# Kernel tuning notes

Measured on AMD Instinct MI355X. Metric: run time of the kernel, lower is better.

## Reference

```python
import jax, jax.numpy as jnp
import numpy as np

B, D, I = 16384, 2048, 2048


def setup_inputs() -> dict:
    key = jax.random.key(0)
    kx, kh, kw = jax.random.split(key, 3)
    x = jax.random.normal(kx, (B, I), dtype=jnp.float32)
    h = jax.random.normal(kh, (B, D), dtype=jnp.float32)
    # input projection weight (Linear, no bias): [d_model, inpt_size]
    W_ih = jax.random.normal(kw, (D, I), dtype=jnp.float32) * 0.02
    # orthogonal-ish hidden transition (torch uses an SVD-orthogonal block),
    # well-conditioned so the inverse is exact and stable
    rng = np.random.default_rng(0)
    q, _ = np.linalg.qr(rng.standard_normal((D, D)).astype(np.float64))
    W_hh = jnp.asarray(q, dtype=jnp.float32)
    W_inv = jnp.asarray(np.linalg.inv(q), dtype=jnp.float32)  # buffer self.inv
    return {"x": x, "h": h, "W_ih": W_ih, "W_hh": W_hh, "W_inv": W_inv}


def reference(x, h, W_ih, W_hh, W_inv):
    # outs = inpt_linear(x) : [B, D]
    outs = jnp.einsum("bi,di->bd", x, W_ih)
    not_trig = outs[..., -1] >= -1.0          # [B]
    h_last = h[..., -1]                        # [B]
    m_fwd = ((h_last > 0) & not_trig)[..., None]   # forward rotation branch
    m_inv = ((h_last < 0) & not_trig)[..., None]   # inverse rotation branch
    m_pass = (~not_trig)[..., None]                # passthrough branch
    hW = h @ W_hh   # torch.matmul(h, weight_hh) (no transpose)
    hI = h @ W_inv  # torch.matmul(h, inv)
    zero = jnp.zeros((), dtype=outs.dtype)
    return (outs
            + jnp.where(m_fwd, hW, zero)
            + jnp.where(m_inv, hI, zero)
            + jnp.where(m_pass, h, zero))
```

## Files before the change

kernel.cpp:

```cpp
#include <hip/hip_runtime.h>
#include <hip/hip_bf16.h>
#include <stdint.h>

#define B_ROWS 16384
#define DIM 2048
#define BK 64
#define NT 96

typedef float f32x4 __attribute__((ext_vector_type(4)));
typedef short bf16x8 __attribute__((ext_vector_type(8)));
using u16 = unsigned short;
using u32 = unsigned int;

__device__ __forceinline__ u32 pack_bf2(float a, float b) {
  __hip_bfloat162 t = __float22bfloat162_rn(float2{a, b});
  union { __hip_bfloat162 b2; u32 u; } cv;
  cv.b2 = t;
  return cv.u;
}

__device__ __forceinline__ u16 f2bf_rne(float f) {
  union { float f; u32 u; } v;
  v.f = f;
  u32 u = v.u;
  u32 r = u + 0x7FFFu + ((u >> 16) & 1u);
  return (u16)(r >> 16);
}

__device__ __forceinline__ void gload16(const void* g, void* l) {
  __builtin_amdgcn_global_load_lds(
      (const __attribute__((address_space(1))) u32*)g,
      (__attribute__((address_space(3))) u32*)l, 16, 0, 0);
}

__global__ __launch_bounds__(256) void k_prep(
    const float* __restrict__ x, const float* __restrict__ h,
    const float* __restrict__ W_ih, int* __restrict__ flags,
    u16* __restrict__ xb, u16* __restrict__ hF, u16* __restrict__ hI) {
  int row = blockIdx.x * 4 + (threadIdx.x >> 6);
  int lane = threadIdx.x & 63;
  const float* xr = x + (size_t)row * DIM;
  const float* hr = h + (size_t)row * DIM;
  const float* wr = W_ih + (size_t)(DIM - 1) * DIM;
  u16* xbr = xb + (size_t)row * DIM;
  double s = 0.0;
  u32 hp[16];
#pragma unroll
  for (int i = 0; i < 8; ++i) {
    int idx = (i * 64 + lane) * 4;
    f32x4 xv = *(const f32x4*)(xr + idx);
    f32x4 wv = *(const f32x4*)(wr + idx);
    f32x4 hv = *(const f32x4*)(hr + idx);
    s += (double)xv.x * wv.x + (double)xv.y * wv.y +
         (double)xv.z * wv.z + (double)xv.w * wv.w;
    *(uint2*)(xbr + idx) = uint2{pack_bf2(xv.x, xv.y), pack_bf2(xv.z, xv.w)};
    hp[2 * i] = pack_bf2(hv.x, hv.y);
    hp[2 * i + 1] = pack_bf2(hv.z, hv.w);
  }
#pragma unroll
  for (int off = 32; off > 0; off >>= 1) s += __shfl_xor(s, off);
  float hl = hr[DIM - 1];
  int f = (s < -1.0) ? 2 : (hl > 0.f ? 0 : (hl < 0.f ? 1 : 3));
  if (lane == 0) flags[row] = f;
  uint2 z{0u, 0u};
  u16* hFr = hF + (size_t)row * DIM;
  u16* hIr = hI + (size_t)row * DIM;
#pragma unroll
  for (int i = 0; i < 8; ++i) {
    int idx = (i * 64 + lane) * 4;
    uint2 p{hp[2 * i], hp[2 * i + 1]};
    *(uint2*)(hFr + idx) = (f == 0) ? p : z;
    *(uint2*)(hIr + idx) = (f == 1) ? p : z;
  }
}

__global__ __launch_bounds__(256) void k_flags_fb(
    const float* __restrict__ x, const float* __restrict__ h,
    const float* __restrict__ W_ih, int* __restrict__ flags) {
  int row = blockIdx.x * 4 + (threadIdx.x >> 6);
  int lane = threadIdx.x & 63;
  const float* xr = x + (size_t)row * DIM;
  const float* wr = W_ih + (size_t)(DIM - 1) * DIM;
  double s = 0.0;
#pragma unroll
  for (int i = 0; i < 8; ++i) {
    int idx = (i * 64 + lane) * 4;
    f32x4 xv = *(const f32x4*)(xr + idx);
    f32x4 wv = *(const f32x4*)(wr + idx);
    s += (double)xv.x * wv.x + (double)xv.y * wv.y +
         (double)xv.z * wv.z + (double)xv.w * wv.w;
  }
#pragma unroll
  for (int off = 32; off > 0; off >>= 1) s += __shfl_xor(s, off);
  if (lane == 0) {
    float hl = h[(size_t)row * DIM + (DIM - 1)];
    flags[row] = (s < -1.0) ? 2 : (hl > 0.f ? 0 : (hl < 0.f ? 1 : 3));
  }
}

__global__ __launch_bounds__(256) void k_convert(const float* __restrict__ src,
                                                 u16* __restrict__ dst) {
  size_t i = ((size_t)blockIdx.x * 256 + threadIdx.x) * 4;
  f32x4 v = *(const f32x4*)(src + i);
  *(uint2*)(dst + i) = uint2{pack_bf2(v.x, v.y), pack_bf2(v.z, v.w)};
}

__global__ __launch_bounds__(256) void k_transpose(const float* __restrict__ src,
                                                   u16* __restrict__ dst) {
  __shared__ float tile[32][33];
  int k0 = blockIdx.x * 32;
  int n0 = blockIdx.y * 32;
  int tx = threadIdx.x & 31;
  int ty = threadIdx.x >> 5;
#pragma unroll
  for (int i = 0; i < 4; ++i)
    tile[ty + 8 * i][tx] = src[(size_t)(k0 + ty + 8 * i) * DIM + n0 + tx];
  __syncthreads();
#pragma unroll
  for (int i = 0; i < 4; ++i)
    dst[(size_t)(n0 + ty + 8 * i) * DIM + k0 + tx] = f2bf_rne(tile[tx][ty + 8 * i]);
}

__global__ __launch_bounds__(512, 2) void k_gemm8(
    const u16* __restrict__ xb, const u16* __restrict__ hF,
    const u16* __restrict__ hI, const u16* __restrict__ Wih,
    const u16* __restrict__ WhhT, const u16* __restrict__ WinvT,
    const int* __restrict__ flags, const float* __restrict__ h,
    float* __restrict__ out) {
  __shared__ __attribute__((aligned(128))) char smem[131072];

  int o = blockIdx.x;
  int brow = (o >> 3) * 256;
  int bcol = (o & 7) * 256;

  int t = threadIdx.x;
  int lane = t & 63;
  int wave = t >> 6;
  int wr = wave >> 2;
  int wc = wave & 3;

  int sx16 = (((lane & 3) ^ ((lane >> 3) & 3)) << 4);
  int fA = (((lane >> 4) ^ ((lane >> 1) & 3)) << 4);
  int arowbase = wr * 128 + (lane & 15);
  int browbase = wc * 64 + (lane & 15);

  auto stage = [&](int T, int isB, int kk) {
    if (T >= NT) T -= NT;
    int seg = T >> 5;
    int kt = T & 31;
    const u16* mat = isB ? (seg == 0 ? Wih : seg == 1 ? WhhT : WinvT)
                         : (seg == 0 ? xb : seg == 1 ? hF : hI);
    int r0 = isB ? bcol : brow;
    size_t gb = (size_t)(r0 + wave * 32 + (lane >> 2)) * (DIM * 2) +
                (size_t)kt * 128 + (size_t)kk * 64 + (size_t)sx16;
    char* ldst = smem + ((T & 1) << 16) + kk * 32768 + isB * 16384 +
                 (wave * 32) * 64;
    gload16((const char*)mat + gb, ldst);
    gload16((const char*)mat + gb + (size_t)16 * (DIM * 2), ldst + 1024);
  };

  f32x4 acc[8][4] = {};
  bf16x8 aF[8], bF[4];

  stage(0, 0, 0); stage(0, 1, 0);
  stage(0, 0, 1); stage(0, 1, 1);
  stage(1, 0, 0); stage(1, 1, 0);
  asm volatile("s_waitcnt vmcnt(8)" ::: "memory");
  __builtin_amdgcn_s_barrier();

#define PHASE(KK, STT, STKK)                                                   \
  {                                                                            \
    const char* Ab_ = smem + buf + (KK) * 32768;                               \
    _Pragma("unroll") for (int m = 0; m < 4; ++m) {                            \
      aF[m] = *(const bf16x8*)(Ab_ + (arowbase + m * 16) * 64 + fA);           \
      aF[4 + m] = *(const bf16x8*)(Ab_ + (arowbase + 64 + m * 16) * 64 + fA);  \
    }                                                                          \
    _Pragma("unroll") for (int n = 0; n < 4; ++n)                              \
        bF[n] = *(const bf16x8*)(Ab_ + 16384 + (browbase + n * 16) * 64 + fA); \
    stage(STT, 0, STKK);                                                       \
    stage(STT, 1, STKK);                                                       \
    asm volatile("s_waitcnt vmcnt(8)" ::: "memory");                           \
    __builtin_amdgcn_s_barrier();                                              \
    asm volatile("s_waitcnt lgkmcnt(0)" ::: "memory");                         \
    __builtin_amdgcn_sched_barrier(0);                                         \
    __builtin_amdgcn_s_setprio(1);                                             \
    _Pragma("unroll") for (int mh = 0; mh < 2; ++mh)                           \
        _Pragma("unroll") for (int m = 0; m < 4; ++m)                          \
            _Pragma("unroll") for (int n = 0; n < 4; ++n)                      \
                acc[mh * 4 + m][n] = __builtin_amdgcn_mfma_f32_16x16x32_bf16(  \
                    aF[mh * 4 + m], bF[n], acc[mh * 4 + m][n], 0, 0, 0);       \
    __builtin_amdgcn_s_setprio(0);                                             \
  }

#pragma unroll 1
  for (int T = 0; T < NT; ++T) {
    const int buf = (T & 1) << 16;
    PHASE(0, T + 1, 1)
    PHASE(1, T + 2, 0)
  }
#undef PHASE
  asm volatile("s_waitcnt vmcnt(0)" ::: "memory");

#pragma unroll
  for (int mi = 0; mi < 8; ++mi) {
    int rbase = brow + wr * 128 + (mi >> 2) * 64 + (mi & 3) * 16 + (lane >> 4) * 4;
#pragma unroll
    for (int j = 0; j < 4; ++j) {
      int row = rbase + j;
      bool pass = (flags[row] == 2);
#pragma unroll
      for (int n = 0; n < 4; ++n) {
        int col = bcol + wc * 64 + n * 16 + (lane & 15);
        float v = acc[mi][n][j];
        if (pass) v += h[(size_t)row * DIM + col];
        out[(size_t)row * DIM + col] = v;
      }
    }
  }
}

#define BM 128
#define BN 128
__global__ __launch_bounds__(256, 2) void k_gemm_fb(
    const float* __restrict__ x, const float* __restrict__ h,
    const u16* __restrict__ Wih, const u16* __restrict__ WhhT,
    const u16* __restrict__ WinvT, const int* __restrict__ flags,
    float* __restrict__ out) {
  __shared__ char smem[(BM + BN) * BK * 2];
  char* sA = smem;
  char* sB = smem + BM * BK * 2;

  int o = blockIdx.x;
  int swz = (o & 7) * ((int)gridDim.x >> 3) + (o >> 3);
  int brow = (swz >> 4) * BM;
  int bcol = (swz & 15) * BN;

  int t = threadIdx.x;
  int lane = t & 63;
  int wave = t >> 6;
  int wrow = (wave >> 1) * 64;
  int wcol = (wave & 1) * 64;

  f32x4 acc[4][4] = {};
  int sc = t & 15;
  int sr0 = t >> 4;

  int aOff[4][2], bOff[4][2];
#pragma unroll
  for (int m = 0; m < 4; ++m)
#pragma unroll
    for (int kk = 0; kk < 2; ++kk) {
      int ar = wrow + m * 16 + (lane & 15);
      aOff[m][kk] = ar * (BK * 2) + ((kk * 64 + (lane >> 4) * 16) ^ ((ar & 7) << 4));
      int br = wcol + m * 16 + (lane & 15);
      bOff[m][kk] = br * (BK * 2) + ((kk * 64 + (lane >> 4) * 16) ^ ((br & 7) << 4));
    }

#pragma unroll 1
  for (int seg = 0; seg < 3; ++seg) {
    const float* Asrc = (seg == 0) ? x : h;
    const u16* Bsrc = (seg == 0) ? Wih : (seg == 1) ? WhhT : WinvT;
    int want = seg - 1;

    float rmask[8];
#pragma unroll
    for (int i = 0; i < 8; ++i) {
      int r = sr0 + 16 * i;
      rmask[i] = (want < 0 || flags[brow + r] == want) ? 1.f : 0.f;
    }

#pragma unroll 1
    for (int k0 = 0; k0 < DIM; k0 += BK) {
      __syncthreads();
#pragma unroll
      for (int i = 0; i < 8; ++i) {
        int r = sr0 + 16 * i;
        f32x4 v = *(const f32x4*)(Asrc + (size_t)(brow + r) * DIM + k0 + sc * 4);
        float msk = rmask[i];
        int off = r * (BK * 2) + ((sc * 8) ^ ((r & 7) << 4));
        *(uint2*)(sA + off) =
            uint2{pack_bf2(v.x * msk, v.y * msk), pack_bf2(v.z * msk, v.w * msk)};
      }
#pragma unroll
      for (int i = 0; i < 4; ++i) {
        int ch = t + 256 * i;
        int r = ch >> 3;
        int c = ch & 7;
        uint4 v = *(const uint4*)(Bsrc + (size_t)(bcol + r) * DIM + k0 + c * 8);
        int off = r * (BK * 2) + ((c * 16) ^ ((r & 7) << 4));
        *(uint4*)(sB + off) = v;
      }
      __syncthreads();
      bf16x8 aF2[4][2], bF2[4][2];
#pragma unroll
      for (int m = 0; m < 4; ++m)
#pragma unroll
        for (int kk = 0; kk < 2; ++kk) {
          aF2[m][kk] = *(const bf16x8*)(sA + aOff[m][kk]);
          bF2[m][kk] = *(const bf16x8*)(sB + bOff[m][kk]);
        }
#pragma unroll
      for (int kk = 0; kk < 2; ++kk)
#pragma unroll
        for (int m = 0; m < 4; ++m)
#pragma unroll
          for (int n = 0; n < 4; ++n)
            acc[m][n] = __builtin_amdgcn_mfma_f32_16x16x32_bf16(
                aF2[m][kk], bF2[n][kk], acc[m][n], 0, 0, 0);
    }
  }

#pragma unroll
  for (int m = 0; m < 4; ++m) {
    int rbase = brow + wrow + m * 16 + (lane >> 4) * 4;
#pragma unroll
    for (int j = 0; j < 4; ++j) {
      int row = rbase + j;
      bool pass = (flags[row] == 2);
#pragma unroll
      for (int n = 0; n < 4; ++n) {
        int col = bcol + wcol + n * 16 + (lane & 15);
        float v = acc[m][n][j];
        if (pass) v += h[(size_t)row * DIM + col];
        out[(size_t)row * DIM + col] = v;
      }
    }
  }
}

extern "C" void kernel_launch(void* const* d_in, const int* in_sizes, int n_in,
                              void* d_out, int out_size, void* d_ws, size_t ws_size,
                              hipStream_t stream) {
  const float* x = (const float*)d_in[0];
  const float* h = (const float*)d_in[1];
  const float* W_ih = (const float*)d_in[2];
  const float* W_hh = (const float*)d_in[3];
  const float* W_inv = (const float*)d_in[4];
  float* out = (float*)d_out;

  char* ws = (char*)d_ws;
  int* flags = (int*)ws;
  u16* WihB = (u16*)(ws + (64 << 10));
  u16* WhhT = WihB + (size_t)DIM * DIM;
  u16* WinvT = WhhT + (size_t)DIM * DIM;
  u16* xb = WinvT + (size_t)DIM * DIM;
  u16* hF = xb + (size_t)B_ROWS * DIM;
  u16* hI = hF + (size_t)B_ROWS * DIM;
  size_t need = (size_t)(64 << 10) + 3ull * DIM * DIM * 2 + 3ull * B_ROWS * DIM * 2;

  k_convert<<<(DIM * DIM / 4) / 256, 256, 0, stream>>>(W_ih, WihB);
  k_transpose<<<dim3(DIM / 32, DIM / 32), 256, 0, stream>>>(W_hh, WhhT);
  k_transpose<<<dim3(DIM / 32, DIM / 32), 256, 0, stream>>>(W_inv, WinvT);

  if (ws_size >= need) {
    k_prep<<<B_ROWS / 4, 256, 0, stream>>>(x, h, W_ih, flags, xb, hF, hI);
    k_gemm8<<<(B_ROWS / 256) * (DIM / 256), 512, 0, stream>>>(
        xb, hF, hI, WihB, WhhT, WinvT, flags, h, out);
  } else {
    k_flags_fb<<<B_ROWS / 4, 256, 0, stream>>>(x, h, W_ih, flags);
    k_gemm_fb<<<(B_ROWS / BM) * (DIM / BN), 256, 0, stream>>>(x, h, WihB, WhhT,
                                                              WinvT, flags, out);
  }
}
```

Baseline: 518.2 us.

## Shrink GEMM tile to 256x128 with 4 waves and triple-buffered K=32 phases

Changes the main GEMM from 512-thread 256x256 tiles with double-buffered K=64 stages to 256-thread 256x128 tiles. Each phase now stages K=32 slices into a 3-deep LDS ring of 24KB buffers. It also adds a block-index swizzle so neighbouring blocks share row or column panels. The aim is smaller LDS use (72KB) to allow two blocks per CU, plus more blocks for load balance, at the cost of lower per-tile arithmetic intensity and more global re-reads of the A operand.

```diff
diff --git a/kernel.cpp b/kernel.cpp
--- a/kernel.cpp
+++ b/kernel.cpp
@@ -4,8 +4,7 @@
 
 #define B_ROWS 16384
 #define DIM 2048
-#define BK 64
-#define NT 96
+#define NPH 192
 
 typedef float f32x4 __attribute__((ext_vector_type(4)));
 typedef short bf16x8 __attribute__((ext_vector_type(8)));
@@ -121,89 +120,92 @@
     dst[(size_t)(n0 + ty + 8 * i) * DIM + k0 + tx] = f2bf_rne(tile[tx][ty + 8 * i]);
 }
 
-__global__ __launch_bounds__(512, 2) void k_gemm8(
+__global__ __launch_bounds__(256, 2) void k_gemm8(
     const u16* __restrict__ xb, const u16* __restrict__ hF,
     const u16* __restrict__ hI, const u16* __restrict__ Wih,
     const u16* __restrict__ WhhT, const u16* __restrict__ WinvT,
     const int* __restrict__ flags, const float* __restrict__ h,
     float* __restrict__ out) {
-  __shared__ __attribute__((aligned(128))) char smem[131072];
+  __shared__ __attribute__((aligned(128))) char smem[73728];
 
   int o = blockIdx.x;
-  int brow = (o >> 3) * 256;
-  int bcol = (o & 7) * 256;
+  int swz = (o & 7) * 128 + (o >> 3);
+  int brow = (swz >> 4) * 256;
+  int bcol = (swz & 15) * 128;
 
   int t = threadIdx.x;
   int lane = t & 63;
   int wave = t >> 6;
-  int wr = wave >> 2;
-  int wc = wave & 3;
+  int wr = wave >> 1;
+  int wc = wave & 1;
 
   int sx16 = (((lane & 3) ^ ((lane >> 3) & 3)) << 4);
   int fA = (((lane >> 4) ^ ((lane >> 1) & 3)) << 4);
   int arowbase = wr * 128 + (lane & 15);
   int browbase = wc * 64 + (lane & 15);
 
-  auto stage = [&](int T, int isB, int kk) {
-    if (T >= NT) T -= NT;
-    int seg = T >> 5;
-    int kt = T & 31;
-    const u16* mat = isB ? (seg == 0 ? Wih : seg == 1 ? WhhT : WinvT)
-                         : (seg == 0 ? xb : seg == 1 ? hF : hI);
-    int r0 = isB ? bcol : brow;
-    size_t gb = (size_t)(r0 + wave * 32 + (lane >> 2)) * (DIM * 2) +
-                (size_t)kt * 128 + (size_t)kk * 64 + (size_t)sx16;
-    char* ldst = smem + ((T & 1) << 16) + kk * 32768 + isB * 16384 +
-                 (wave * 32) * 64;
-    gload16((const char*)mat + gb, ldst);
-    gload16((const char*)mat + gb + (size_t)16 * (DIM * 2), ldst + 1024);
+  auto stage = [&](int T, int p) {
+    if (T >= NPH) T -= NPH;
+    int seg = T >> 6;
+    int kt = (T >> 1) & 31;
+    int kk = T & 1;
+    const u16* Am = seg == 0 ? xb : (seg == 1 ? hF : hI);
+    const u16* Bm = seg == 0 ? Wih : (seg == 1 ? WhhT : WinvT);
+    size_t kb = (size_t)kt * 128 + (size_t)kk * 64 + (size_t)sx16;
+    char* pb = smem + p * 24576;
+#pragma unroll
+    for (int i = 0; i < 4; ++i) {
+      int r = brow + wave * 64 + i * 16 + (lane >> 2);
+      gload16((const char*)Am + (size_t)r * (DIM * 2) + kb,
+              pb + wave * 4096 + i * 1024);
+    }
+#pragma unroll
+    for (int i = 0; i < 2; ++i) {
+      int r = bcol + wave * 32 + i * 16 + (lane >> 2);
+      gload16((const char*)Bm + (size_t)r * (DIM * 2) + kb,
+              pb + 16384 + wave * 2048 + i * 1024);
+    }
   };
 
   f32x4 acc[8][4] = {};
   bf16x8 aF[8], bF[4];
 
-  stage(0, 0, 0); stage(0, 1, 0);
-  stage(0, 0, 1); stage(0, 1, 1);
-  stage(1, 0, 0); stage(1, 1, 0);
-  asm volatile("s_waitcnt vmcnt(8)" ::: "memory");
+  stage(0, 0);
+  stage(1, 1);
+  asm volatile("s_waitcnt vmcnt(6)" ::: "memory");
   __builtin_amdgcn_s_barrier();
 
-#define PHASE(KK, STT, STKK)                                                   \
-  {                                                                            \
-    const char* Ab_ = smem + buf + (KK) * 32768;                               \
-    _Pragma("unroll") for (int m = 0; m < 4; ++m) {                            \
-      aF[m] = *(const bf16x8*)(Ab_ + (arowbase + m * 16) * 64 + fA);           \
-      aF[4 + m] = *(const bf16x8*)(Ab_ + (arowbase + 64 + m * 16) * 64 + fA);  \
-    }                                                                          \
-    _Pragma("unroll") for (int n = 0; n < 4; ++n)                              \
-        bF[n] = *(const bf16x8*)(Ab_ + 16384 + (browbase + n * 16) * 64 + fA); \
-    stage(STT, 0, STKK);                                                       \
-    stage(STT, 1, STKK);                                                       \
-    asm volatile("s_waitcnt vmcnt(8)" ::: "memory");                           \
-    __builtin_amdgcn_s_barrier();                                              \
-    asm volatile("s_waitcnt lgkmcnt(0)" ::: "memory");                         \
-    __builtin_amdgcn_sched_barrier(0);                                         \
-    __builtin_amdgcn_s_setprio(1);                                             \
-    _Pragma("unroll") for (int mh = 0; mh < 2; ++mh)                           \
-        _Pragma("unroll") for (int m = 0; m < 4; ++m)                          \
-            _Pragma("unroll") for (int n = 0; n < 4; ++n)                      \
-                acc[mh * 4 + m][n] = __builtin_amdgcn_mfma_f32_16x16x32_bf16(  \
-                    aF[mh * 4 + m], bF[n], acc[mh * 4 + m][n], 0, 0, 0);       \
-    __builtin_amdgcn_s_setprio(0);                                             \
-  }
-
+  int pcur = 0;
 #pragma unroll 1
-  for (int T = 0; T < NT; ++T) {
-    const int buf = (T & 1) << 16;
-    PHASE(0, T + 1, 1)
-    PHASE(1, T + 2, 0)
-  }
-#undef PHASE
+  for (int P = 0; P < NPH; ++P) {
+    const char* pb = smem + pcur * 24576;
+#pragma unroll
+    for (int m = 0; m < 8; ++m)
+      aF[m] = *(const bf16x8*)(pb + (arowbase + m * 16) * 64 + fA);
+#pragma unroll
+    for (int n = 0; n < 4; ++n)
+      bF[n] = *(const bf16x8*)(pb + 16384 + (browbase + n * 16) * 64 + fA);
+    int pst = pcur + 2; if (pst >= 3) pst -= 3;
+    stage(P + 2, pst);
+    asm volatile("s_waitcnt vmcnt(6)" ::: "memory");
+    __builtin_amdgcn_s_barrier();
+    asm volatile("s_waitcnt lgkmcnt(0)" ::: "memory");
+    __builtin_amdgcn_sched_barrier(0);
+    __builtin_amdgcn_s_setprio(1);
+#pragma unroll
+    for (int m = 0; m < 8; ++m)
+#pragma unroll
+      for (int n = 0; n < 4; ++n)
+        acc[m][n] = __builtin_amdgcn_mfma_f32_16x16x32_bf16(
+            aF[m], bF[n], acc[m][n], 0, 0, 0);
+    __builtin_amdgcn_s_setprio(0);
+    pcur = (pcur == 2) ? 0 : pcur + 1;
+  }
   asm volatile("s_waitcnt vmcnt(0)" ::: "memory");
 
 #pragma unroll
   for (int mi = 0; mi < 8; ++mi) {
-    int rbase = brow + wr * 128 + (mi >> 2) * 64 + (mi & 3) * 16 + (lane >> 4) * 4;
+    int rbase = brow + wr * 128 + mi * 16 + (lane >> 4) * 4;
 #pragma unroll
     for (int j = 0; j < 4; ++j) {
       int row = rbase + j;
@@ -221,6 +223,7 @@
 
 #define BM 128
 #define BN 128
+#define BK 64
 __global__ __launch_bounds__(256, 2) void k_gemm_fb(
     const float* __restrict__ x, const float* __restrict__ h,
     const u16* __restrict__ Wih, const u16* __restrict__ WhhT,
@@ -354,7 +357,7 @@
 
   if (ws_size >= need) {
     k_prep<<<B_ROWS / 4, 256, 0, stream>>>(x, h, W_ih, flags, xb, hF, hI);
-    k_gemm8<<<(B_ROWS / 256) * (DIM / 256), 512, 0, stream>>>(
+    k_gemm8<<<(B_ROWS / 256) * (DIM / 128), 256, 0, stream>>>(
         xb, hF, hI, WihB, WhhT, WinvT, flags, h, out);
   } else {
     k_flags_fb<<<B_ROWS / 4, 256, 0, stream>>>(x, h, W_ih, flags);
```

Result: slower. 769.2 us (+48.4%).
